# Kernel tuning notes

Measured on AMD Instinct MI355X. Metric: run time of the kernel, lower is better.

## Reference

```python
import jax, jax.numpy as jnp
import numpy as np


def setup_inputs() -> dict:
    key = jax.random.key(0)
    ks = jax.random.split(key, 8)
    B, C, H, W = 4, 256, 64, 64
    s = 1.0 / np.sqrt(C)
    return {
        "x": jax.random.normal(ks[0], (B, C, H, W), jnp.float32),
        "y": jax.random.normal(ks[1], (B, C, H, W), jnp.float32),
        "Wq": jax.random.normal(ks[2], (C, C), jnp.float32) * s,
        "bq": jax.random.normal(ks[3], (C,), jnp.float32) * 0.01,
        "Wk": jax.random.normal(ks[4], (C, C), jnp.float32) * s,
        "bk": jax.random.normal(ks[5], (C,), jnp.float32) * 0.01,
        "Wv": jax.random.normal(ks[6], (C, C), jnp.float32) * s,
        "bv": jax.random.normal(ks[7], (C,), jnp.float32) * 0.01,
    }


def reference(x, y, Wq, bq, Wk, bk, Wv, bv):
    B, C, H, W = x.shape
    N = H * W
    # 1x1 convs == per-pixel linear over channels. Flatten spatial to N.
    xf = x.reshape(B, C, N)  # [B,C,N]
    yf = y.reshape(B, C, N)
    # q: [B,N,C]; k: [B,C,N]; v: [B,N,C]
    q = jnp.einsum('oc,bcn->bno', Wq, xf) + bq[None, None, :]
    k = jnp.einsum('oc,bcn->bon', Wk, yf) + bk[None, :, None]
    v = jnp.einsum('oc,bcn->bno', Wv, yf) + bv[None, None, :]
    # attention scores [B,N,N]; NOTE: original has no 1/sqrt(d) scaling.
    attn = jax.nn.softmax(jnp.einsum('bnc,bcm->bnm', q, k), axis=-1)
    out = jnp.einsum('bnm,bmc->bnc', attn, v)  # [B,N,C]
    return out.transpose(0, 2, 1).reshape(B, C, H, W)
```

## Files before the change

### kernel.cpp

```cpp
#include <hip/hip_runtime.h>


typedef __attribute__((ext_vector_type(8))) short short8;
typedef __attribute__((ext_vector_type(4))) float f32x4;
typedef __attribute__((ext_vector_type(4))) int int4v;
typedef __attribute__((ext_vector_type(8))) _Float16 half8;

#define LOG2E 1.44269504089f

static __device__ __forceinline__ float exp2_fast(float x){ return __builtin_amdgcn_exp2f(x); }

static __device__ __forceinline__ int pk_f16(float a, float b){
  auto h = __builtin_amdgcn_cvt_pkrtz(a, b);
  return __builtin_bit_cast(int, h);
}
static __device__ __forceinline__ unsigned short f2h(float v){
  return __builtin_bit_cast(unsigned short, (_Float16)v);
}

#define GLOAD16(gp, lp) __builtin_amdgcn_global_load_lds( \
  (const __attribute__((address_space(1))) void*)(gp),    \
  (__attribute__((address_space(3))) void*)(lp), 16, 0, 0)

#define MFMAF16(a,b,c) __builtin_amdgcn_mfma_f32_16x16x32_f16( \
  __builtin_bit_cast(half8, a), __builtin_bit_cast(half8, b), c, 0, 0, 0)

__global__ __launch_bounds__(256) void cvt_w(
    const float* __restrict__ wq, const float* __restrict__ wk,
    const float* __restrict__ wv, unsigned short* __restrict__ wf)
{
  const int o = blockIdx.x, t = blockIdx.y, c = threadIdx.x;
  const float* w = (t == 0) ? wq : ((t == 1) ? wk : wv);
  wf[t*65536 + o*256 + c] = f2h(w[o*256 + c]);
}

__global__ __launch_bounds__(256, 2) void proj_kernel(
    const float* __restrict__ x, const float* __restrict__ y,
    const unsigned short* __restrict__ wf,
    const float* __restrict__ bq, const float* __restrict__ bk, const float* __restrict__ bv,
    unsigned short* __restrict__ qf, unsigned short* __restrict__ kf,
    unsigned short* __restrict__ vtf)
{
  __shared__ float xs[256*64];
  __shared__ short wlds[2][4096];

  const int t   = blockIdx.z;
  const int b   = blockIdx.y;
  const int n0  = blockIdx.x * 64;
  const int tid = threadIdx.x;
  const int w   = tid >> 6, lane = tid & 63, g = lane >> 4, l15 = lane & 15;

  const float* src = ((t == 0) ? x : y) + (size_t)b*1048576 + n0;
  const char*  wt_b = (const char*)(wf + t*65536);

  int wsrc[2];
  #pragma unroll
  for (int i = 0; i < 2; i++){
    int s = w*2 + i;
    int row = s*2 + (lane >> 5);
    wsrc[i] = row*512 + (((lane & 31)*16) ^ ((row & 7) << 4));
  }

  #pragma unroll
  for (int i = 0; i < 16; i++){
    int c  = i*16 + (tid >> 4);
    int gg = (c >> 3) & 3;
    int sg = ((tid & 15) - 4*gg) & 15;
    GLOAD16((const char*)src + (size_t)c*16384 + sg*16,
            (char*)xs + (i*256 + tid)*16);
  }
  #pragma unroll
  for (int i = 0; i < 2; i++){
    int s = w*2 + i;
    GLOAD16(wt_b + wsrc[i], (char*)&wlds[0][0] + s*1024);
  }
  __syncthreads();

  int4v xf[8];
  {
    const int nn = (w*16 + l15 + 16*g) & 63;
    #pragma unroll
    for (int cs = 0; cs < 8; cs++){
      float v[8];
      #pragma unroll
      for (int j = 0; j < 8; j++) v[j] = xs[(cs*32 + g*8 + j)*64 + nn];
      int4v f;
      f[0] = pk_f16(v[0], v[1]); f[1] = pk_f16(v[2], v[3]);
      f[2] = pk_f16(v[4], v[5]); f[3] = pk_f16(v[6], v[7]);
      xf[cs] = f;
    }
  }

  const float* bias = (t == 0) ? bq : ((t == 1) ? bk : bv);

  int buf = 0;
  for (int ot = 0; ot < 16; ot++){
    if (ot < 15){
      #pragma unroll
      for (int i = 0; i < 2; i++){
        int s = w*2 + i;
        GLOAD16(wt_b + (ot+1)*8192 + wsrc[i], (char*)&wlds[buf^1][0] + s*1024);
      }
    }

    f32x4 acc;
    if (t < 2){
      float bo = bias[ot*16 + l15];
      acc = (f32x4){bo, bo, bo, bo};
    } else {
      acc = *(const f32x4*)&bias[ot*16 + g*4];
    }
    const char* wb = (const char*)&wlds[buf][0];
    #pragma unroll
    for (int cs = 0; cs < 8; cs++){
      short8 wfr = *(const short8*)(wb + (l15*512 + ((cs*64 + g*16) ^ ((l15 & 7) << 4))));
      if (t < 2) acc = MFMAF16(__builtin_bit_cast(short8, xf[cs]), wfr, acc);
      else       acc = MFMAF16(wfr, __builtin_bit_cast(short8, xf[cs]), acc);
    }
    if (t < 2){
      unsigned short* outp = (t == 0) ? qf : kf;
      #pragma unroll
      for (int r = 0; r < 4; r++){
        int n = n0 + w*16 + g*4 + r;
        outp[((size_t)(b*4096 + n))*256 + ot*16 + l15] = f2h(acc[r]);
      }
    } else {
      #pragma unroll
      for (int r = 0; r < 4; r++){
        int o = ot*16 + g*4 + r;
        vtf[((size_t)(b*256 + o))*4096 + n0 + w*16 + l15] = f2h(acc[r]);
      }
    }
    __syncthreads();
    buf ^= 1;
  }
}

__global__ __launch_bounds__(512, 2) void attn_kernel(
    const unsigned short* __restrict__ qf, const unsigned short* __restrict__ kf,
    const unsigned short* __restrict__ vtf,
    float* __restrict__ outp, unsigned short* __restrict__ part,
    float* __restrict__ mlbuf, int nsplit, int iters)
{
  __shared__ short k_s[3*32*256];
  __shared__ short v_s[3*256*32];

  const int tid  = threadIdx.x;
  const int w    = tid >> 6, lane = tid & 63, g = lane >> 4, col = lane & 15;
  const int bid  = blockIdx.x;

  int b, kvq, qt;
  if (nsplit == 4){
    int xcd = bid & 7, s = bid >> 3;
    int combo = xcd*2 + (s >> 4);
    qt = s & 15;  b = combo >> 2;  kvq = combo & 3;
  } else {
    int combo = bid & 7;
    qt = bid >> 3;  b = combo >> 1;  kvq = combo & 1;
  }
  const int qbase = qt * 256;

  short8 qh[2][8];
  #pragma unroll
  for (int nn = 0; nn < 2; nn++){
    const size_t qoff = ((size_t)(b*4096 + qbase + w*32 + nn*16 + col))*256 + g*8;
    #pragma unroll
    for (int ch = 0; ch < 8; ch++)
      qh[nn][ch] = *(const short8*)(qf + qoff + ch*32);
  }

  f32x4 o_acc[2][16];
  #pragma unroll
  for (int nn = 0; nn < 2; nn++)
    #pragma unroll
    for (int i = 0; i < 16; i++){
      o_acc[nn][i][0]=0.f; o_acc[nn][i][1]=0.f; o_acc[nn][i][2]=0.f; o_acc[nn][i][3]=0.f;
    }
  float mst[2] = {-1e30f, -1e30f};
  float lst[2] = {0.f, 0.f};

  const int swzK = (col & 7) << 4;
  const int g16  = g << 4;
  const int kb0  = col * 512;
  const int kb1  = kb0 + 8192;
  const int vb   = col*64 + (g16 ^ (((col>>1)&3)<<4));

  const int laneA  = col + ((g & 1) ? 32 : 0);
  const int laneB  = laneA + 16;
  const bool selLow = (g < 2);

  int ksrc[2], vsrc[2];
  #pragma unroll
  for (int i = 0; i < 2; i++){
    int s = w*2 + i;
    int m = s*2 + (lane >> 5);
    ksrc[i] = m*512 + (((lane & 31)*16) ^ ((m & 7) << 4));
    int c = s*16 + (lane >> 2);
    vsrc[i] = c*8192 + (((lane & 3)*16) ^ (((lane >> 3) & 3) << 4));
  }

  const int rows = 4096 / nsplit;
  const char* khg = (const char*)(kf + ((size_t)b*4096 + kvq*rows)*256);
  const char* vg  = (const char*)(vtf + ((size_t)b*256)*4096) + kvq*rows*2;

  #pragma unroll
  for (int i = 0; i < 2; i++){
    int s = w*2 + i;
    GLOAD16(khg + ksrc[i], (char*)k_s + s*1024);
    GLOAD16(vg  + vsrc[i], (char*)v_s + s*1024);
  }

  int cur = 0, nxt = 1;
  for (int it = 0; it < iters; ++it){
    if (it + 1 < iters){
      const char* kht = khg + (size_t)(it+1)*16384;
      const char* vtt = vg  + (size_t)(it+1)*64;
      const int ko = nxt*16384, vo = nxt*16384;
      #pragma unroll
      for (int i = 0; i < 2; i++){
        int s = w*2 + i;
        GLOAD16(kht + ksrc[i], (char*)k_s + ko + s*1024);
        GLOAD16(vtt + vsrc[i], (char*)v_s + vo + s*1024);
      }
      asm volatile("s_waitcnt vmcnt(4)" ::: "memory");
    } else {
      asm volatile("s_waitcnt vmcnt(0)" ::: "memory");
    }
    __builtin_amdgcn_s_barrier();
    __builtin_amdgcn_sched_barrier(0);

    const char* kb   = (const char*)k_s + cur*16384;
    const char* vbuf = (const char*)v_s + cur*16384;

    f32x4 s00 = {0.f,0.f,0.f,0.f}, s01 = {0.f,0.f,0.f,0.f};
    f32x4 s10 = {0.f,0.f,0.f,0.f}, s11 = {0.f,0.f,0.f,0.f};
    __builtin_amdgcn_s_setprio(1);
    #pragma unroll
    for (int ch = 0; ch < 8; ch++){
      int inr = ((ch << 6) | g16) ^ swzK;
      short8 kh0 = *(const short8*)(kb + kb0 + inr);
      short8 kh1 = *(const short8*)(kb + kb1 + inr);
      s00 = MFMAF16(kh0, qh[0][ch], s00);
      s01 = MFMAF16(kh1, qh[0][ch], s01);
      s10 = MFMAF16(kh0, qh[1][ch], s10);
      s11 = MFMAF16(kh1, qh[1][ch], s11);
    }
    __builtin_amdgcn_s_setprio(0);

    short8 pf[2];
    #pragma unroll
    for (int nn = 0; nn < 2; nn++){
      f32x4 s0 = nn ? s10 : s00;
      f32x4 s1 = nn ? s11 : s01;
      float tmax = fmaxf(fmaxf(fmaxf(s0[0],s0[1]), fmaxf(s0[2],s0[3])),
                         fmaxf(fmaxf(s1[0],s1[1]), fmaxf(s1[2],s1[3])));
      tmax = fmaxf(tmax, __shfl_xor(tmax, 16));
      tmax = fmaxf(tmax, __shfl_xor(tmax, 32));

      if (__any(tmax > mst[nn])){
        float mn = fmaxf(mst[nn], tmax);
        float sc = exp2_fast((mst[nn] - mn) * LOG2E);
        lst[nn] *= sc;
        #pragma unroll
        for (int i = 0; i < 16; i++){
          o_acc[nn][i][0]*=sc; o_acc[nn][i][1]*=sc;
          o_acc[nn][i][2]*=sc; o_acc[nn][i][3]*=sc;
        }
        mst[nn] = mn;
      }
      const float mb = mst[nn] * LOG2E;
      float p0 = exp2_fast(s0[0]*LOG2E - mb);
      float p1 = exp2_fast(s0[1]*LOG2E - mb);
      float p2 = exp2_fast(s0[2]*LOG2E - mb);
      float p3 = exp2_fast(s0[3]*LOG2E - mb);
      float p4 = exp2_fast(s1[0]*LOG2E - mb);
      float p5 = exp2_fast(s1[1]*LOG2E - mb);
      float p6 = exp2_fast(s1[2]*LOG2E - mb);
      float p7 = exp2_fast(s1[3]*LOG2E - mb);

      float psum = ((p0+p1)+(p2+p3)) + ((p4+p5)+(p6+p7));
      psum += __shfl_xor(psum, 16);
      psum += __shfl_xor(psum, 32);
      lst[nn] += psum;

      int W0 = pk_f16(p0, p1);
      int W1 = pk_f16(p2, p3);
      int W2 = pk_f16(p4, p5);
      int W3 = pk_f16(p6, p7);

      int a0 = __shfl(W0, laneA), a1 = __shfl(W1, laneA);
      int a2 = __shfl(W2, laneA), a3 = __shfl(W3, laneA);
      int b0 = __shfl(W0, laneB), b1 = __shfl(W1, laneB);
      int b2 = __shfl(W2, laneB), b3 = __shfl(W3, laneB);
      int4v ti;
      ti[0] = selLow ? a0 : a2;
      ti[1] = selLow ? a1 : a3;
      ti[2] = selLow ? b0 : b2;
      ti[3] = selLow ? b1 : b3;
      pf[nn] = __builtin_bit_cast(short8, ti);
    }

    __builtin_amdgcn_s_setprio(1);
    #pragma unroll
    for (int ct = 0; ct < 16; ct++){
      short8 vf = *(const short8*)(vbuf + ct*1024 + vb);
      o_acc[0][ct] = MFMAF16(vf, pf[0], o_acc[0][ct]);
      o_acc[1][ct] = MFMAF16(vf, pf[1], o_acc[1][ct]);
    }
    __builtin_amdgcn_s_setprio(0);

    cur = nxt;
    nxt = (nxt + 1 == 3) ? 0 : nxt + 1;
  }

  #pragma unroll
  for (int nn = 0; nn < 2; nn++){
    const int n = qbase + w*32 + nn*16 + col;
    if (kvq == 0){
      #pragma unroll
      for (int ct = 0; ct < 16; ct++)
        #pragma unroll
        for (int r = 0; r < 4; r++){
          int c = ct*16 + g*4 + r;
          outp[((size_t)(b*256 + c))*4096 + n] = o_acc[nn][ct][r];
        }
    } else {
      const size_t pbase = ((size_t)((kvq-1)*1024 + b*256))*4096;
      #pragma unroll
      for (int ct = 0; ct < 16; ct++)
        #pragma unroll
        for (int r = 0; r < 4; r++){
          int c = ct*16 + g*4 + r;
          part[pbase + (size_t)c*4096 + n] = f2h(o_acc[nn][ct][r]);
        }
    }
    if (g == 0){
      const size_t mb2 = ((size_t)(kvq*4 + b)*4096 + n)*2;
      mlbuf[mb2]     = mst[nn];
      mlbuf[mb2 + 1] = lst[nn];
    }
  }
}

__global__ __launch_bounds__(256) void merge_kernel(
    const unsigned short* __restrict__ part, const float* __restrict__ mlbuf,
    float* __restrict__ out, int nsplit)
{
  const int T    = blockIdx.x*256 + threadIdx.x;
  const int rowc = T >> 9;
  const int n8   = (T & 511) * 8;
  const int b    = rowc >> 8;

  float num[8], den[8], m[8];
  {
    f32x4 a0 = *(const f32x4*)&out[(size_t)rowc*4096 + n8];
    f32x4 a1 = *(const f32x4*)&out[(size_t)rowc*4096 + n8 + 4];
    const float* mlp = &mlbuf[((size_t)b*4096 + n8)*2];
    #pragma unroll
    for (int j = 0; j < 8; j++){
      m[j]   = mlp[j*2];
      den[j] = mlp[j*2 + 1];
      num[j] = (j < 4) ? a0[j] : a1[j-4];
    }
  }
  for (int s = 1; s < nsplit; s++){
    short8 pv = *(const short8*)&part[((size_t)((s-1)*1024 + rowc))*4096 + n8];
    const float* mlp = &mlbuf[((size_t)(s*4 + b)*4096 + n8)*2];
    #pragma unroll
    for (int j = 0; j < 8; j++){
      float ms = mlp[j*2], ls = mlp[j*2 + 1];
      unsigned short u = (unsigned short)pv[j];
      float ps = (float)*(const _Float16*)&u;
      float mn = fmaxf(m[j], ms);
      float sa = exp2_fast((m[j] - mn) * LOG2E);
      float sb = exp2_fast((ms   - mn) * LOG2E);
      num[j] = num[j]*sa + ps*sb;
      den[j] = den[j]*sa + ls*sb;
      m[j] = mn;
    }
  }
  f32x4 o0, o1;
  #pragma unroll
  for (int j = 0; j < 8; j++){
    float v = num[j] / den[j];
    if (j < 4) o0[j] = v; else o1[j-4] = v;
  }
  float* op = out + (size_t)rowc*4096 + n8;
  *(f32x4*)op       = o0;
  *(f32x4*)(op + 4) = o1;
}

extern "C" void kernel_launch(void* const* d_in, const int* in_sizes, int n_in,
                              void* d_out, int out_size, void* d_ws, size_t ws_size,
                              hipStream_t stream)
{
  const float* x  = (const float*)d_in[0];
  const float* y  = (const float*)d_in[1];
  const float* Wq = (const float*)d_in[2];
  const float* bq = (const float*)d_in[3];
  const float* Wk = (const float*)d_in[4];
  const float* bk = (const float*)d_in[5];
  const float* Wv = (const float*)d_in[6];
  const float* bv = (const float*)d_in[7];
  float* out = (float*)d_out;

  char* ws = (char*)d_ws;
  const size_t MB = 1048576;
  unsigned short* qf   = (unsigned short*)(ws + 0*MB);
  unsigned short* kfp  = (unsigned short*)(ws + 8*MB);
  unsigned short* vtf  = (unsigned short*)(ws + 16*MB);
  unsigned short* wf   = (unsigned short*)(ws + 24*MB);
  unsigned short* part = (unsigned short*)(ws + 24*MB + 393216);

  const int nsplit = (ws_size >= 50*MB) ? 4 : 2;
  const int iters  = (4096 / nsplit) / 32;
  float* mlb = (float*)(ws + 24*MB + 393216 + (size_t)(nsplit-1)*8*MB);

  cvt_w<<<dim3(256,3), dim3(256), 0, stream>>>(Wq, Wk, Wv, wf);
  proj_kernel<<<dim3(64,4,3), dim3(256), 0, stream>>>(x, y, wf, bq, bk, bv,
                                                      qf, kfp, vtf);
  attn_kernel<<<dim3(64*nsplit), dim3(512), 0, stream>>>(qf, kfp, vtf, out, part,
                                                         mlb, nsplit, iters);
  merge_kernel<<<dim3(2048), dim3(256), 0, stream>>>(part, mlb, out, nsplit);
}
```

Before: 159.7 us.

## Triple-buffer projection weights, defer rescale, normalize partials before merge

The projection kernel moves to a three-deep weight buffer with explicit vmcnt waits and barriers. Its output stores are deferred until after all 16 output tiles are accumulated in registers. The attention kernel skips the online-softmax rescale unless the new max exceeds the running max by more than 8, and normalizes partial outputs by 1/l before storing them. The merge kernel is adjusted to match, and attention launch bounds change to one block per SM. These changes aim to cut rescale work and synchronisation stalls, but they raise register pressure and risk fp16 overflow in the unnormalised accumulators.

```diff
diff --git a/kernel.cpp b/kernel.cpp
--- a/kernel.cpp
+++ b/kernel.cpp
@@ -42,7 +42,7 @@
     unsigned short* __restrict__ vtf)
 {
   __shared__ float xs[256*64];
-  __shared__ short wlds[2][4096];
+  __shared__ short wlds[3][4096];
 
   const int t   = blockIdx.z;
   const int b   = blockIdx.y;
@@ -93,50 +93,60 @@
 
   const float* bias = (t == 0) ? bq : ((t == 1) ? bk : bv);
 
-  int buf = 0;
+  f32x4 acc[16];
+  #pragma unroll
   for (int ot = 0; ot < 16; ot++){
     if (ot < 15){
       #pragma unroll
       for (int i = 0; i < 2; i++){
         int s = w*2 + i;
-        GLOAD16(wt_b + (ot+1)*8192 + wsrc[i], (char*)&wlds[buf^1][0] + s*1024);
+        GLOAD16(wt_b + (ot+1)*8192 + wsrc[i], (char*)&wlds[(ot+1)%3][0] + s*1024);
       }
-    }
-
-    f32x4 acc;
+      asm volatile("s_waitcnt vmcnt(2)" ::: "memory");
+    } else {
+      asm volatile("s_waitcnt vmcnt(0)" ::: "memory");
+    }
+    __builtin_amdgcn_s_barrier();
+    __builtin_amdgcn_sched_barrier(0);
+
+    f32x4 a;
     if (t < 2){
       float bo = bias[ot*16 + l15];
-      acc = (f32x4){bo, bo, bo, bo};
+      a = (f32x4){bo, bo, bo, bo};
     } else {
-      acc = *(const f32x4*)&bias[ot*16 + g*4];
-    }
-    const char* wb = (const char*)&wlds[buf][0];
+      a = *(const f32x4*)&bias[ot*16 + g*4];
+    }
+    const char* wb = (const char*)&wlds[ot%3][0];
     #pragma unroll
     for (int cs = 0; cs < 8; cs++){
       short8 wfr = *(const short8*)(wb + (l15*512 + ((cs*64 + g*16) ^ ((l15 & 7) << 4))));
-      if (t < 2) acc = MFMAF16(__builtin_bit_cast(short8, xf[cs]), wfr, acc);
-      else       acc = MFMAF16(wfr, __builtin_bit_cast(short8, xf[cs]), acc);
-    }
-    if (t < 2){
-      unsigned short* outp = (t == 0) ? qf : kf;
+      if (t < 2) a = MFMAF16(__builtin_bit_cast(short8, xf[cs]), wfr, a);
+      else       a = MFMAF16(wfr, __builtin_bit_cast(short8, xf[cs]), a);
+    }
+    acc[ot] = a;
+  }
+
+  if (t < 2){
+    unsigned short* outp = (t == 0) ? qf : kf;
+    #pragma unroll
+    for (int ot = 0; ot < 16; ot++)
       #pragma unroll
       for (int r = 0; r < 4; r++){
         int n = n0 + w*16 + g*4 + r;
-        outp[((size_t)(b*4096 + n))*256 + ot*16 + l15] = f2h(acc[r]);
+        outp[((size_t)(b*4096 + n))*256 + ot*16 + l15] = f2h(acc[ot][r]);
       }
-    } else {
+  } else {
+    #pragma unroll
+    for (int ot = 0; ot < 16; ot++)
       #pragma unroll
       for (int r = 0; r < 4; r++){
         int o = ot*16 + g*4 + r;
-        vtf[((size_t)(b*256 + o))*4096 + n0 + w*16 + l15] = f2h(acc[r]);
+        vtf[((size_t)(b*256 + o))*4096 + n0 + w*16 + l15] = f2h(acc[ot][r]);
       }
-    }
-    __syncthreads();
-    buf ^= 1;
-  }
-}
-
-__global__ __launch_bounds__(512, 2) void attn_kernel(
+  }
+}
+
+__global__ __launch_bounds__(512, 1) void attn_kernel(
     const unsigned short* __restrict__ qf, const unsigned short* __restrict__ kf,
     const unsigned short* __restrict__ vtf,
     float* __restrict__ outp, unsigned short* __restrict__ part,
@@ -203,25 +213,24 @@
   const char* khg = (const char*)(kf + ((size_t)b*4096 + kvq*rows)*256);
   const char* vg  = (const char*)(vtf + ((size_t)b*256)*4096) + kvq*rows*2;
 
-  #pragma unroll
-  for (int i = 0; i < 2; i++){
-    int s = w*2 + i;
-    GLOAD16(khg + ksrc[i], (char*)k_s + s*1024);
-    GLOAD16(vg  + vsrc[i], (char*)v_s + s*1024);
-  }
+#define STAGE_TILE(T, BSEL) do {                                   \
+    const char* kht_ = khg + (size_t)(T)*16384;                    \
+    const char* vtt_ = vg  + (size_t)(T)*64;                       \
+    const int off_ = (BSEL)*16384;                                 \
+    _Pragma("unroll")                                              \
+    for (int i_ = 0; i_ < 2; i_++){                                \
+      int s_ = w*2 + i_;                                           \
+      GLOAD16(kht_ + ksrc[i_], (char*)k_s + off_ + s_*1024);       \
+      GLOAD16(vtt_ + vsrc[i_], (char*)v_s + off_ + s_*1024);       \
+    }                                                              \
+  } while (0)
+
+  STAGE_TILE(0, 0);
 
   int cur = 0, nxt = 1;
   for (int it = 0; it < iters; ++it){
     if (it + 1 < iters){
-      const char* kht = khg + (size_t)(it+1)*16384;
-      const char* vtt = vg  + (size_t)(it+1)*64;
-      const int ko = nxt*16384, vo = nxt*16384;
-      #pragma unroll
-      for (int i = 0; i < 2; i++){
-        int s = w*2 + i;
-        GLOAD16(kht + ksrc[i], (char*)k_s + ko + s*1024);
-        GLOAD16(vtt + vsrc[i], (char*)v_s + vo + s*1024);
-      }
+      STAGE_TILE(it + 1, nxt);
       asm volatile("s_waitcnt vmcnt(4)" ::: "memory");
     } else {
       asm volatile("s_waitcnt vmcnt(0)" ::: "memory");
@@ -257,7 +266,7 @@
       tmax = fmaxf(tmax, __shfl_xor(tmax, 16));
       tmax = fmaxf(tmax, __shfl_xor(tmax, 32));
 
-      if (__any(tmax > mst[nn])){
+      if (__any(tmax > mst[nn] + 8.f)){
         float mn = fmaxf(mst[nn], tmax);
         float sc = exp2_fast((mst[nn] - mn) * LOG2E);
         lst[nn] *= sc;
@@ -312,17 +321,19 @@
     cur = nxt;
     nxt = (nxt + 1 == 3) ? 0 : nxt + 1;
   }
+#undef STAGE_TILE
 
   #pragma unroll
   for (int nn = 0; nn < 2; nn++){
     const int n = qbase + w*32 + nn*16 + col;
+    const float rl = 1.0f / lst[nn];
     if (kvq == 0){
       #pragma unroll
       for (int ct = 0; ct < 16; ct++)
         #pragma unroll
         for (int r = 0; r < 4; r++){
           int c = ct*16 + g*4 + r;
-          outp[((size_t)(b*256 + c))*4096 + n] = o_acc[nn][ct][r];
+          outp[((size_t)(b*256 + c))*4096 + n] = o_acc[nn][ct][r] * rl;
         }
     } else {
       const size_t pbase = ((size_t)((kvq-1)*1024 + b*256))*4096;
@@ -331,7 +342,7 @@
         #pragma unroll
         for (int r = 0; r < 4; r++){
           int c = ct*16 + g*4 + r;
-          part[pbase + (size_t)c*4096 + n] = f2h(o_acc[nn][ct][r]);
+          part[pbase + (size_t)c*4096 + n] = f2h(o_acc[nn][ct][r] * rl);
         }
     }
     if (g == 0){
@@ -360,7 +371,7 @@
     for (int j = 0; j < 8; j++){
       m[j]   = mlp[j*2];
       den[j] = mlp[j*2 + 1];
-      num[j] = (j < 4) ? a0[j] : a1[j-4];
+      num[j] = ((j < 4) ? a0[j] : a1[j-4]) * den[j];
     }
   }
   for (int s = 1; s < nsplit; s++){
@@ -374,7 +385,7 @@
       float mn = fmaxf(m[j], ms);
       float sa = exp2_fast((m[j] - mn) * LOG2E);
       float sb = exp2_fast((ms   - mn) * LOG2E);
-      num[j] = num[j]*sa + ps*sb;
+      num[j] = num[j]*sa + ps*ls*sb;
       den[j] = den[j]*sa + ls*sb;
       m[j] = mn;
     }
```

Result: slower. 163.7 us (+2.5%).
